# Optimization experiments

Measured on AMD Instinct MI355X. Metric: run time of the kernel, lower is better.

The kernel has to match this reference:

```python
import jax, jax.numpy as jnp
import numpy as np
from jax.scipy.linalg import solve_triangular

LS = 0.5414            # frozen GP length scale (_gp_scale.data = 0.5414)
L2 = LS * LS
D = 2
K_OPS = D + 2          # operators: identity, d/dx_i (i=1..d), laplacian
JITTER_KXX = 1e-5
JITTER_AKA = 1e-4
JITTER_YY = 1e-5


def _opiK(xout, xin, l2, d):
    # op_i applied to first arg of RBF kernel -> (bs, k, m, n)
    r = xout[:, :, None, :] - xin[:, None, :, :]            # (bs,m,n,d)
    u = jnp.sum(r * r, axis=-1) / l2                        # (bs,m,n)
    K = jnp.exp(-0.5 * u)
    ri = jnp.moveaxis(r, -1, 1)                             # (bs,d,m,n)
    grad = -(ri / l2) * K[:, None]                          # d/dx_i K
    lap = ((u - d) / l2) * K                                # Lap_x K
    return jnp.concatenate([K[:, None], grad, lap[:, None]], axis=1)


def _opiKopjfull(x, l2, d):
    # op_i on first arg, op_j on second arg -> (bs, k, k, m, m)
    r = x[:, :, None, :] - x[:, None, :, :]
    u = jnp.sum(r * r, axis=-1) / l2
    K = jnp.exp(-0.5 * u)
    ri = jnp.moveaxis(r, -1, 1)                             # (bs,d,m,m)
    gK = (ri / l2) * K[:, None]                             # d/dy_j K
    lapK = ((u - d) / l2) * K                               # Lap K (either arg)
    eye = jnp.eye(d, dtype=x.dtype)[None, :, :, None, None]
    gg = (eye / l2 - ri[:, :, None] * ri[:, None] / (l2 * l2)) * K[:, None, None]  # d/dx_i d/dy_j K
    glap = (ri / (l2 * l2)) * (((2.0 + d - u) * K)[:, None])  # d/dx_i Lap_y K
    laplap = (((u - d) ** 2 - 4.0 * u + 2.0 * d) / (l2 * l2)) * K  # Lap_x Lap_y K
    row0 = jnp.concatenate([K[:, None, None], gK[:, None], lapK[:, None, None]], axis=2)
    rowg = jnp.concatenate([(-gK)[:, :, None], gg, glap[:, :, None]], axis=2)
    rowl = jnp.concatenate([lapK[:, None, None], (-glap)[:, None], laplap[:, None, None]], axis=2)
    return jnp.concatenate([row0, rowg, rowl], axis=1)


def _psd_solve(L, B):
    # (Kxx + jitter I)^{-1} B via Cholesky (stands in for gpytorch inv_matmul/CG)
    y = solve_triangular(L, B, lower=True)
    return solve_triangular(L, y, lower=True, trans=1)


def _forward(xin, meanin, Kin, weight, bias):
    bs, n, c = meanin.shape
    d, k, l2 = D, K_OPS, L2
    xout, m = xin, n
    r = xin[:, :, None, :] - xin[:, None, :, :]
    Kxx = jnp.exp(-0.5 * jnp.sum(r * r, axis=-1) / l2)      # (bs,n,n)
    In = jnp.eye(n, dtype=xin.dtype)
    Lc = jnp.linalg.cholesky(Kxx + JITTER_KXX * In)
    opiKmn = _opiK(xout, xin, l2, d)                        # (bs,k,m,n)
    # posterior mean of op_i applied to the GP
    opimean = (opiKmn.reshape(bs, k * m, n) @ _psd_solve(Lc, meanin)).reshape(bs, k, m, c)
    Amean = jnp.transpose(opimean, (0, 2, 3, 1)).reshape(bs, m, c * k) @ weight.T + bias
    W = weight.reshape(-1, c, k)                            # (cout,c,k)
    W2 = jnp.einsum('oci,ocj->ij', W, W) / W.shape[0]       # (k,k)
    Kxxinvopi = jnp.swapaxes(
        _psd_solve(Lc, jnp.swapaxes(opiKmn.reshape(bs, k * m, n), 1, 2)), 1, 2)  # (bs,km,n)
    interp_weights = jnp.swapaxes(_psd_solve(Lc, Kin), 1, 2)                      # (bs,n,n)
    opi_interp = jnp.transpose((Kxxinvopi @ interp_weights).reshape(bs, k, m, n), (0, 2, 3, 1))  # (bs,m,n,k)
    Ak_interp = (opi_interp @ W2).reshape(bs, m, n * k)
    Im = jnp.eye(m, dtype=xin.dtype)
    AkinA = Ak_interp @ jnp.transpose(opiKmn, (0, 3, 1, 2)).reshape(bs, n * k, m) + JITTER_AKA * Im
    opiKxxxopj = jnp.transpose(
        (Kxxinvopi @ jnp.swapaxes(opiKmn.reshape(bs, k * m, n), 1, 2)).reshape(bs, k, m, k, m),
        (0, 1, 3, 2, 4))                                    # (bs,k,k,m,m)
    ijkyy = _opiKopjfull(xout, l2, d) - opiKxxxopj          # posterior cov of op_i f, op_j f
    AkAyy = jnp.einsum('bijmp,ij->bmp', ijkyy, W2) + JITTER_YY * Im
    full_AKA = AkinA + AkAyy
    return (xout, Amean, full_AKA)


def setup_inputs() -> dict:
    bs, n, cin, cout = 4, 576, 32, 64
    key = jax.random.key(0)
    k1, k2, k3, k4, k5 = jax.random.split(key, 5)
    xin = jax.random.uniform(k1, (bs, n, D), dtype=jnp.float32) * 6.0
    meanin = jax.random.normal(k2, (bs, n, cin), dtype=jnp.float32)
    A = jax.random.normal(k3, (bs, n, n), dtype=jnp.float32) / np.float32(np.sqrt(n))
    Kin = A @ jnp.swapaxes(A, 1, 2) + 0.1 * jnp.eye(n, dtype=jnp.float32)  # PSD covariance
    fan_in = cin * K_OPS
    weight = jax.random.normal(k4, (cout, fan_in), dtype=jnp.float32) / np.float32(np.sqrt(fan_in))
    bias = jax.random.normal(k5, (cout,), dtype=jnp.float32) * 0.01
    return {"xin": xin, "meanin": meanin, "Kin": Kin, "weight": weight, "bias": bias}


def reference(xin, meanin, Kin, weight, bias):
    return _forward(xin, meanin, Kin, weight, bias)
```

## Files before the change

kernel.cpp:

```cpp
#include <hip/hip_runtime.h>
#include <math.h>

#define NPTS 576
#define N2 331776
#define BSZ 4
#define NB 64
#define NT 9

#define INVL2 (1.0f/0.29311396f)

typedef __attribute__((ext_vector_type(8))) short short8v;
typedef __attribute__((ext_vector_type(16))) float f32x16;

__global__ void build_k(const float* __restrict__ xin,
                        float* __restrict__ Kxx, float* __restrict__ opiK,
                        float* __restrict__ out,
                        const float* __restrict__ w, float* __restrict__ W2) {
    int idx = blockIdx.x * 256 + threadIdx.x;
    if (idx < 4608) out[idx] = xin[idx];
    int b = idx / N2;
    int rem = idx - b * N2;
    int m = rem / NPTS;
    int nn = rem - m * NPTS;
    const float* xb = xin + (size_t)b * NPTS * 2;
// ... 87 lines not shown
                }
            }
            float tii = __shfl(tcol[i], base + i);
            v[i] = s / tii;
        }
        #pragma unroll
        for (int i = 0; i < 16; ++i) V[base + i][base + c] = v[i];
    }
    __syncthreads();
    const int PI[6] = {1,2,3,2,3,3};
    const int PJ[6] = {0,1,2,0,1,0};
    int rr16 = tid >> 4, cc16 = tid & 15;
    for (int p = 0; p < 6; ++p) {
        int I = PI[p], J = PJ[p];
        float s = 0.0f;
        for (int K = J; K < I; ++K)
            #pragma unroll
            for (int t = 0; t < 16; ++t)
                s += T[I*16+rr16][K*16+t] * V[K*16+t][J*16+cc16];
        tmp[rr16][cc16] = s;
        __syncthreads();
        float s2 = 0.0f;
        for (int t = 0; t <= rr16; ++t) s2 += V[I*16+rr16][I*16+t] * tmp[t][cc16];
        __syncthreads();
        V[I*16+rr16][J*16+cc16] = -s2;
        __syncthreads();
    }
}

__global__ void chol_diag0(const float* __restrict__ A, float* __restrict__ LinvKK) {
    int b = blockIdx.x;
    const float* Ab = A + (size_t)b * N2;
    __shared__ float T[NB][NB+1];
    __shared__ float V[NB][NB+1];
    __shared__ float tmp[16][17];
    int tid = threadIdx.x;
    for (int idx = tid; idx < NB*NB; idx += 256) {
        int r = idx >> 6, c = idx & 63;
        T[r][c] = Ab[(size_t)r * NPTS + c];
        V[r][c] = 0.0f;
    }
    __syncthreads();
    factor_invert_64(T, V, tmp, tid);
    float* Vg = LinvKK + (size_t)b * NT * NB * NB;
    for (int idx = tid; idx < NB*NB; idx += 256) Vg[idx] = V[idx >> 6][idx & 63];
}

__global__ __launch_bounds__(256)
void chol_step(float* __restrict__ A, float* __restrict__ LL,
               float* __restrict__ LinvKK, int kb) {
    int b = blockIdx.y;
    int p = blockIdx.x;
    int ir = 0;
    while (p >= ir + 1) { p -= ir + 1; ir++; }
    int ib = kb + 1 + ir, jb = kb + 1 + p;
    float* Ab = A + (size_t)b * N2;
    float* LLb = LL + (size_t)b * N2;
    __shared__ float Ai[NB][NB+1];
    __shared__ float Aj[NB][NB+1];
    __shared__ float Vs[NB][NB+1];
    __shared__ float tmp[16][17];
    int tid = threadIdx.x;
    int tx = tid & 15, ty = tid >> 4;
    const float* Vg = LinvKK + ((size_t)b * NT + kb) * NB * NB;
    bool diag = (ib == jb);
    for (int idx = tid; idx < NB*NB; idx += 256) {
        int r = idx >> 6, c = idx & 63;
        Ai[r][c] = Ab[(size_t)(ib*NB + r) * NPTS + kb*NB + c];
        Aj[r][c] = diag ? 0.0f : Ab[(size_t)(jb*NB + r) * NPTS + kb*NB + c];
        Vs[r][c] = Vg[idx];
    }
    float U[4][4];
    #pragma unroll
    for (int i = 0; i < 4; ++i)
        #pragma unroll
        for (int j = 0; j < 4; ++j)
            U[i][j] = Ab[(size_t)(ib*NB + ty*4+i) * NPTS + jb*NB + tx*4+j];
    __syncthreads();
    float Li[4][4] = {}, Lj[4][4] = {};
    for (int k = 0; k < NB; ++k) {
        float a[4], v[4];
        #pragma unroll
        for (int i = 0; i < 4; ++i) a[i] = Ai[ty*4+i][k];
        #pragma unroll
        for (int j = 0; j < 4; ++j) v[j] = Vs[tx*4+j][k];
        #pragma unroll
        for (int i = 0; i < 4; ++i)
            #pragma unroll
            for (int j = 0; j < 4; ++j) Li[i][j] += a[i] * v[j];
        if (!diag) {
            float aj[4];
            #pragma unroll
            for (int i = 0; i < 4; ++i) aj[i] = Aj[ty*4+i][k];
            #pragma unroll
            for (int i = 0; i < 4; ++i)
                #pragma unroll
                for (int j = 0; j < 4; ++j) Lj[i][j] += aj[i] * v[j];
        }
    }
    __syncthreads();
    #pragma unroll
    for (int i = 0; i < 4; ++i)
        #pragma unroll
        for (int j = 0; j < 4; ++j) {
            Ai[ty*4+i][tx*4+j] = Li[i][j];
            Aj[ty*4+i][tx*4+j] = diag ? Li[i][j] : Lj[i][j];
        }
    if (diag) {
        #pragma unroll
        for (int i = 0; i < 4; ++i)
            #pragma unroll
            for (int j = 0; j < 4; ++j)
                LLb[(size_t)(ib*NB + ty*4+i) * NPTS + kb*NB + tx*4+j] = Li[i][j];
    }
    __syncthreads();
    float s[4][4] = {};
    for (int k = 0; k < NB; ++k) {
        float a[4], v[4];
        #pragma unroll
        for (int i = 0; i < 4; ++i) a[i] = Ai[ty*4+i][k];
        #pragma unroll
        for (int j = 0; j < 4; ++j) v[j] = Aj[tx*4+j][k];
        #pragma unroll
        for (int i = 0; i < 4; ++i)
            #pragma unroll
            for (int j = 0; j < 4; ++j) s[i][j] += a[i] * v[j];
    }
    #pragma unroll
    for (int i = 0; i < 4; ++i)
        #pragma unroll
        for (int j = 0; j < 4; ++j) U[i][j] -= s[i][j];
    if (blockIdx.x != 0) {
        #pragma unroll
        for (int i = 0; i < 4; ++i)
            #pragma unroll
            for (int j = 0; j < 4; ++j)
                Ab[(size_t)(ib*NB + ty*4+i) * NPTS + jb*NB + tx*4+j] = U[i][j];
        return;
    }
    __syncthreads();
    #pragma unroll
    for (int i = 0; i < 4; ++i)
        #pragma unroll
        for (int j = 0; j < 4; ++j) Ai[ty*4+i][tx*4+j] = U[i][j];
    for (int idx = tid; idx < NB*NB; idx += 256) Aj[idx >> 6][idx & 63] = 0.0f;
    __syncthreads();
    factor_invert_64(Ai, Aj, tmp, tid);
    float* Vo = LinvKK + ((size_t)b * NT + (kb + 1)) * NB * NB;
    for (int idx = tid; idx < NB*NB; idx += 256) Vo[idx] = Aj[idx >> 6][idx & 63];
}

__global__ __launch_bounds__(256)
void trinv_blk(const float* __restrict__ L, const float* __restrict__ LinvKK,
               float* __restrict__ Linv) {
    int sp = blockIdx.x, jb = blockIdx.y, b = blockIdx.z;
    const float* Lb = L + (size_t)b * N2;
    float* Xg = Linv + (size_t)b * N2;
    const float* Vg = LinvKK + (size_t)b * NT * NB * NB;
    int c0 = jb * NB + sp * 16;

    __shared__ float LsT[64][72];
    __shared__ float Xc[576][20];
    __shared__ float Ss[64][20];
    __shared__ float Red[4][64][20];

    int tid = threadIdx.x;
    int kq = tid >> 6;
    int rg = (tid >> 2) & 15;
    int cg = tid & 3;
    int sr = tid >> 2, st0 = (tid & 3) * 16;

    float4 pf0, pf1, pf2, pf3;

#define TRINV_ISSUE_L(ibv, kbv)                                               \
    { const float* src_ = Lb + (size_t)((ibv) * NB + sr) * NPTS + (kbv) * NB + st0; \
      pf0 = *(const float4*)(src_ + 0);  pf1 = *(const float4*)(src_ + 4);    \
      pf2 = *(const float4*)(src_ + 8);  pf3 = *(const float4*)(src_ + 12); }

#define TRINV_ISSUE_V(ibv)                                                    \
    { const float* src_ = Vg + (size_t)(ibv) * NB * NB + sr * NB + st0;       \
      pf0 = *(const float4*)(src_ + 0);  pf1 = *(const float4*)(src_ + 4);    \
      pf2 = *(const float4*)(src_ + 8);  pf3 = *(const float4*)(src_ + 12); }

#define TRINV_COMMIT()                                                        \
    { LsT[st0 + 0][sr]  = pf0.x; LsT[st0 + 1][sr]  = pf0.y;                   \
      LsT[st0 + 2][sr]  = pf0.z; LsT[st0 + 3][sr]  = pf0.w;                   \
      LsT[st0 + 4][sr]  = pf1.x; LsT[st0 + 5][sr]  = pf1.y;                   \
      LsT[st0 + 6][sr]  = pf1.z; LsT[st0 + 7][sr]  = pf1.w;                   \
      LsT[st0 + 8][sr]  = pf2.x; LsT[st0 + 9][sr]  = pf2.y;                   \
      LsT[st0 + 10][sr] = pf2.z; LsT[st0 + 11][sr] = pf2.w;                   \
      LsT[st0 + 12][sr] = pf3.x; LsT[st0 + 13][sr] = pf3.y;                   \
      LsT[st0 + 14][sr] = pf3.z; LsT[st0 + 15][sr] = pf3.w; }

    {
        const float* Vjj = Vg + (size_t)jb * NB * NB;
        int r = tid >> 2, c4 = (tid & 3) * 4;
        float4 v = *(const float4*)(Vjj + r * NB + sp * 16 + c4);
        *(float4*)&Xc[r][c4] = v;
        *(float4*)(Xg + (size_t)(jb * NB + r) * NPTS + c0 + c4) = v;
    }
    if (jb + 1 < NT) TRINV_ISSUE_L(jb + 1, jb);
    __syncthreads();

    for (int ib = jb + 1; ib < NT; ++ib) {
        float acc[4][4] = {};
        for (int kb = jb; kb < ib; ++kb) {
            TRINV_COMMIT();
            __syncthreads();
            if (kb + 1 < ib) { TRINV_ISSUE_L(ib, kb + 1); }
            else             { TRINV_ISSUE_V(ib); }
            int xbase = (kb - jb) * 64;
            #pragma unroll
            for (int t = 0; t < 16; ++t) {
                int k = kq * 16 + t;
                float a4[4]; *(float4*)a4 = *(const float4*)&LsT[k][rg * 4];
                float x4[4]; *(float4*)x4 = *(const float4*)&Xc[xbase + k][cg * 4];
                #pragma unroll
                for (int i = 0; i < 4; ++i)
                    #pragma unroll
                    for (int j = 0; j < 4; ++j)
                        acc[i][j] += a4[i] * x4[j];
            }
            __syncthreads();
        }
        TRINV_COMMIT();
        #pragma unroll
        for (int i = 0; i < 4; ++i)
            *(float4*)&Red[kq][rg * 4 + i][cg * 4] = *(float4*)&acc[i][0];
        __syncthreads();
        {
            int r = tid >> 2, c4 = (tid & 3) * 4;
            float4 s0 = *(float4*)&Red[0][r][c4];
            float4 s1 = *(float4*)&Red[1][r][c4];
            float4 s2 = *(float4*)&Red[2][r][c4];
            float4 s3 = *(float4*)&Red[3][r][c4];
            float4 s; s.x = s0.x + s1.x + s2.x + s3.x;
            s.y = s0.y + s1.y + s2.y + s3.y;
            s.z = s0.z + s1.z + s2.z + s3.z;
            s.w = s0.w + s1.w + s2.w + s3.w;
            *(float4*)&Ss[r][c4] = s;
        }
        __syncthreads();
        if (ib + 1 < NT) TRINV_ISSUE_L(ib + 1, jb);
        float acc2[4][4] = {};
        #pragma unroll
        for (int t = 0; t < 16; ++t) {
            int k = kq * 16 + t;
            float a4[4]; *(float4*)a4 = *(const float4*)&LsT[k][rg * 4];
            float s4[4]; *(float4*)s4 = *(const float4*)&Ss[k][cg * 4];
            #pragma unroll
            for (int i = 0; i < 4; ++i)
                #pragma unroll
                for (int j = 0; j < 4; ++j)
                    acc2[i][j] += a4[i] * s4[j];
        }
        __syncthreads();
        #pragma unroll
        for (int i = 0; i < 4; ++i)
            *(float4*)&Red[kq][rg * 4 + i][cg * 4] = *(float4*)&acc2[i][0];
        __syncthreads();
        int obase = (ib - jb) * 64;
        {
            int r = tid >> 2, c4 = (tid & 3) * 4;
            float4 s0 = *(float4*)&Red[0][r][c4];
            float4 s1 = *(float4*)&Red[1][r][c4];
            float4 s2 = *(float4*)&Red[2][r][c4];
            float4 s3 = *(float4*)&Red[3][r][c4];
            float4 s; s.x = -(s0.x + s1.x + s2.x + s3.x);
            s.y = -(s0.y + s1.y + s2.y + s3.y);
            s.z = -(s0.z + s1.z + s2.z + s3.z);
            s.w = -(s0.w + s1.w + s2.w + s3.w);
            *(float4*)&Xc[obase + r][c4] = s;
            *(float4*)(Xg + (size_t)(ib * NB + r) * NPTS + c0 + c4) = s;
        }
        __syncthreads();
    }
#undef TRINV_ISSUE_L
#undef TRINV_ISSUE_V
#undef TRINV_COMMIT
}

__device__ inline void split3(float v, unsigned short& h0, unsigned short& h1,
                              unsigned short& h2) {
    unsigned u0 = __float_as_uint(v) & 0xffff0000u;
    float f0 = __uint_as_float(u0);
    float r1 = v - f0;
    unsigned u1 = __float_as_uint(r1) & 0xffff0000u;
    float f1 = __uint_as_float(u1);
    float r2 = r1 - f1;
    h0 = (unsigned short)(u0 >> 16);
    h1 = (unsigned short)(u1 >> 16);
    h2 = (unsigned short)((__float_as_uint(r2) + 0x8000u) >> 16);
}

__device__ inline void pack_store(unsigned short* dst, const unsigned short* v) {
    uint4 w;
    w.x = (unsigned)v[0] | ((unsigned)v[1] << 16);
    w.y = (unsigned)v[2] | ((unsigned)v[3] << 16);
    w.z = (unsigned)v[4] | ((unsigned)v[5] << 16);
    w.w = (unsigned)v[6] | ((unsigned)v[7] << 16);
    *(uint4*)dst = w;
}

template<int EPIB>
__global__ __launch_bounds__(256, 2)
void mm_p2_mfma(const float* __restrict__ Aall, const float* __restrict__ Ball,
                float* __restrict__ Call, long sA, long sB, long sC)
{
    int id = blockIdx.x;
    int x8 = id & 7, qq = id >> 3;
    int nx = qq % 9;
    int band = x8 + 8 * (qq / 9);
    if (band >= 18 * BSZ) return;
    int t  = band % 18;
    int b  = band / 18;
    int pp = t / 9, my = t % 9;
    const float* A0 = Aall + (size_t)b * sA + (size_t)(pp * 2) * N2;
    const float* A1 = A0 + N2;
    const float* B  = Ball + (size_t)b * sB;
    float* C0 = Call + (size_t)b * sC + (size_t)(pp * 2) * N2;
    float* C1 = C0 + N2;
    int n0 = nx * 64, m0 = my * 64;

    __shared__ __align__(16) unsigned short As[12][2][64][8];
    __shared__ __align__(16) unsigned short Bs[6][2][64][8];

    int tid  = threadIdx.x;
    int lane = tid & 63;
    int wid  = tid >> 6;
    int wr = wid >> 1, wc = wid & 1;

    f32x16 acc0, acc1;
    #pragma unroll
    for (int i = 0; i < 16; ++i) { acc0[i] = 0.0f; acc1[i] = 0.0f; }

    int ap   = tid >> 7;
    int aq   = tid & 127;
    int ar   = aq >> 1;
    int asub = aq & 1;
    const float* Apl = ap ? A1 : A0;
    int areg = ar >> 5;
    int aln  = ar & 31;

    int bc   = tid & 63;
    int bkg  = tid >> 6;
    int bsub = bkg >> 1;
    int bln  = (bc & 31) + 32 * (bkg & 1);
    int bwc  = bc >> 5;

    float av[16];
    float bv[8];

    auto loadA = [&](int k0) {
        const float* p = Apl + (size_t)(m0 + ar) * 576 + k0 + asub * 16;
        float4 t0 = *(const float4*)(p);
        float4 t1 = *(const float4*)(p + 4);
        float4 t2 = *(const float4*)(p + 8);
        float4 t3 = *(const float4*)(p + 12);
        av[0]=t0.x;  av[1]=t0.y;  av[2]=t0.z;  av[3]=t0.w;
        av[4]=t1.x;  av[5]=t1.y;  av[6]=t1.z;  av[7]=t1.w;
        av[8]=t2.x;  av[9]=t2.y;  av[10]=t2.z; av[11]=t2.w;
        av[12]=t3.x; av[13]=t3.y; av[14]=t3.z; av[15]=t3.w;
    };
    auto loadB = [&](int k0) {
        const float* p = B + (size_t)(k0 + bkg * 8) * 576 + n0 + bc;
        #pragma unroll
        for (int j = 0; j < 8; ++j) {
            float v = p[(size_t)j * 576];
            if (EPIB) { if (k0 + bkg * 8 + j == n0 + bc) v -= 1.0f; }
            bv[j] = v;
        }
    };
    auto storeA = [&]() {
        unsigned short s0[16], s1[16], s2[16];
        #pragma unroll
        for (int j = 0; j < 16; ++j) split3(av[j], s0[j], s1[j], s2[j]);
        #pragma unroll
        for (int h = 0; h < 2; ++h) {
            int ln = aln + 32 * h;
            pack_store(&As[(ap*3 + 0)*2 + areg][asub][ln][0], &s0[8*h]);
            pack_store(&As[(ap*3 + 1)*2 + areg][asub][ln][0], &s1[8*h]);
            pack_store(&As[(ap*3 + 2)*2 + areg][asub][ln][0], &s2[8*h]);
        }
    };
    auto storeB = [&]() {
        unsigned short s0[8], s1[8], s2[8];
        #pragma unroll
        for (int j = 0; j < 8; ++j) split3(bv[j], s0[j], s1[j], s2[j]);
        pack_store(&Bs[0*2 + bwc][bsub][bln][0], s0);
        pack_store(&Bs[1*2 + bwc][bsub][bln][0], s1);
        pack_store(&Bs[2*2 + bwc][bsub][bln][0], s2);
    };

    const short8v* Af = (const short8v*)As;
    const short8v* Bf = (const short8v*)Bs;

    loadA(0); loadB(0);
    for (int k0 = 0; k0 < 576; k0 += 32) {
        storeA(); storeB();
        __syncthreads();
        if (k0 + 32 < 576) { loadA(k0 + 32); loadB(k0 + 32); }
        #pragma unroll
        for (int sub = 0; sub < 2; ++sub) {
            short8v b0 = Bf[((0*2 + wc)*2 + sub)*64 + lane];
            short8v b1 = Bf[((1*2 + wc)*2 + sub)*64 + lane];
            short8v b2 = Bf[((2*2 + wc)*2 + sub)*64 + lane];
            short8v a0 = Af[((0*3 + 0)*2 + wr)*128 + sub*64 + lane];
            short8v a1 = Af[((0*3 + 1)*2 + wr)*128 + sub*64 + lane];
            short8v a2 = Af[((0*3 + 2)*2 + wr)*128 + sub*64 + lane];
            acc0 = __builtin_amdgcn_mfma_f32_32x32x16_bf16(a0, b0, acc0, 0, 0, 0);
            acc0 = __builtin_amdgcn_mfma_f32_32x32x16_bf16(a0, b1, acc0, 0, 0, 0);
            acc0 = __builtin_amdgcn_mfma_f32_32x32x16_bf16(a1, b0, acc0, 0, 0, 0);
            acc0 = __builtin_amdgcn_mfma_f32_32x32x16_bf16(a1, b1, acc0, 0, 0, 0);
            acc0 = __builtin_amdgcn_mfma_f32_32x32x16_bf16(a0, b2, acc0, 0, 0, 0);
            acc0 = __builtin_amdgcn_mfma_f32_32x32x16_bf16(a2, b0, acc0, 0, 0, 0);
            a0 = Af[((1*3 + 0)*2 + wr)*128 + sub*64 + lane];
            a1 = Af[((1*3 + 1)*2 + wr)*128 + sub*64 + lane];
            a2 = Af[((1*3 + 2)*2 + wr)*128 + sub*64 + lane];
            acc1 = __builtin_amdgcn_mfma_f32_32x32x16_bf16(a0, b0, acc1, 0, 0, 0);
            acc1 = __builtin_amdgcn_mfma_f32_32x32x16_bf16(a0, b1, acc1, 0, 0, 0);
            acc1 = __builtin_amdgcn_mfma_f32_32x32x16_bf16(a1, b0, acc1, 0, 0, 0);
            acc1 = __builtin_amdgcn_mfma_f32_32x32x16_bf16(a1, b1, acc1, 0, 0, 0);
            acc1 = __builtin_amdgcn_mfma_f32_32x32x16_bf16(a0, b2, acc1, 0, 0, 0);
            acc1 = __builtin_amdgcn_mfma_f32_32x32x16_bf16(a2, b0, acc1, 0, 0, 0);
        }
        __syncthreads();
    }

    int colg = n0 + 32*wc + (lane & 31);
    int rowb = m0 + 32*wr + 4*(lane >> 5);
    #pragma unroll
    for (int reg = 0; reg < 16; ++reg) {
        int row = rowb + (reg & 3) + 8*(reg >> 2);
        C0[(size_t)row * 576 + colg] = acc0[reg];
        C1[(size_t)row * 576 + colg] = acc1[reg];
    }
}

__global__ __launch_bounds__(256, 2)
void mm_abt_mfma(const float* __restrict__ Aall, const float* __restrict__ Ball,
                 float* __restrict__ Call, long sA, long sB, long sC, long sSplit)
{
    int p = blockIdx.x;
    int ir = 0;
    while (p >= ir + 1) { p -= ir + 1; ir++; }
    int my = ir, nx = p;
    int zz = blockIdx.z;
    int sp = zz & 3, b = zz >> 2;
    const float* A = Aall + (size_t)b * sA + (size_t)sp * N2;
    const float* B = Ball + (size_t)b * sB + (size_t)sp * N2;
    float* Cp = Call + (size_t)b * sC + (size_t)sp * sSplit;
    int m0 = my * 64, n0 = nx * 64;

    __shared__ __align__(16) unsigned short Fr[12][2][64][8];

    int tid  = threadIdx.x;
    int lane = tid & 63;
    int wid  = tid >> 6;
    int wr = wid >> 1, wc = wid & 1;

    f32x16 acc;
    #pragma unroll
    for (int i = 0; i < 16; ++i) acc[i] = 0.0f;

    int sel  = tid >> 7;
    int q2   = tid & 127;
    int r    = q2 >> 1;
    int ssub = q2 & 1;
    const float* Src = sel ? B : A;
    int base0 = sel ? n0 : m0;
    int rreg = r >> 5;
    int rln  = r & 31;

    float av[16];

    auto loadF = [&](int k0) {
        const float* pp = Src + (size_t)(base0 + r) * 576 + k0 + ssub * 16;
        float4 t0 = *(const float4*)(pp);
        float4 t1 = *(const float4*)(pp + 4);
        float4 t2 = *(const float4*)(pp + 8);
        float4 t3 = *(const float4*)(pp + 12);
        av[0]=t0.x;  av[1]=t0.y;  av[2]=t0.z;  av[3]=t0.w;
        av[4]=t1.x;  av[5]=t1.y;  av[6]=t1.z;  av[7]=t1.w;
        av[8]=t2.x;  av[9]=t2.y;  av[10]=t2.z; av[11]=t2.w;
        av[12]=t3.x; av[13]=t3.y; av[14]=t3.z; av[15]=t3.w;
    };
    auto storeF = [&]() {
        unsigned short s0[16], s1[16], s2[16];
        #pragma unroll
        for (int j = 0; j < 16; ++j) split3(av[j], s0[j], s1[j], s2[j]);
        #pragma unroll
        for (int h = 0; h < 2; ++h) {
            int ln = rln + 32 * h;
            pack_store(&Fr[sel*6 + 0*2 + rreg][ssub][ln][0], &s0[8*h]);
            pack_store(&Fr[sel*6 + 1*2 + rreg][ssub][ln][0], &s1[8*h]);
            pack_store(&Fr[sel*6 + 2*2 + rreg][ssub][ln][0], &s2[8*h]);
        }
    };

    const short8v* Ff = (const short8v*)Fr;

    loadF(0);
    for (int k0 = 0; k0 < 576; k0 += 32) {
        storeF();
        __syncthreads();
        if (k0 + 32 < 576) loadF(k0 + 32);
        #pragma unroll
        for (int sub = 0; sub < 2; ++sub) {
            short8v a0 = Ff[((0*2 + wr)*2 + sub)*64 + lane];
            short8v a1 = Ff[((1*2 + wr)*2 + sub)*64 + lane];
            short8v a2 = Ff[((2*2 + wr)*2 + sub)*64 + lane];
            short8v b0 = Ff[((6 + 0*2 + wc)*2 + sub)*64 + lane];
            short8v b1 = Ff[((6 + 1*2 + wc)*2 + sub)*64 + lane];
            short8v b2 = Ff[((6 + 2*2 + wc)*2 + sub)*64 + lane];
            acc = __builtin_amdgcn_mfma_f32_32x32x16_bf16(a0, b0, acc, 0, 0, 0);
            acc = __builtin_amdgcn_mfma_f32_32x32x16_bf16(a0, b1, acc, 0, 0, 0);
            acc = __builtin_amdgcn_mfma_f32_32x32x16_bf16(a1, b0, acc, 0, 0, 0);
            acc = __builtin_amdgcn_mfma_f32_32x32x16_bf16(a1, b1, acc, 0, 0, 0);
            acc = __builtin_amdgcn_mfma_f32_32x32x16_bf16(a0, b2, acc, 0, 0, 0);
            acc = __builtin_amdgcn_mfma_f32_32x32x16_bf16(a2, b0, acc, 0, 0, 0);
        }
        __syncthreads();
    }

    int colg = n0 + 32*wc + (lane & 31);
    int rowb = m0 + 32*wr + 4*(lane >> 5);
    #pragma unroll
    for (int reg = 0; reg < 16; ++reg) {
        int row = rowb + (reg & 3) + 8*(reg >> 2);
        Cp[(size_t)row * 576 + colg] = acc[reg];
    }
}

__global__ __launch_bounds__(256, 2)
void mm_ata_mfma(const float* __restrict__ Lg, float* __restrict__ C,
                 long sA, long sC)
{
    int p = blockIdx.x;
    int ir = 0;
    while (p >= ir + 1) { p -= ir + 1; ir++; }
    int my = ir, nx = p;
    int b = blockIdx.z;
    const float* A = Lg + (size_t)b * sA;
    float* Cb = C + (size_t)b * sC;
    int m0 = my * 64, n0 = nx * 64;
    int kBeg = m0;

    __shared__ __align__(16) unsigned short Fr[12][2][64][8];

    int tid  = threadIdx.x;
    int lane = tid & 63;
    int wid  = tid >> 6;
    int wr = wid >> 1, wc = wid & 1;

    f32x16 acc;
    #pragma unroll
    for (int i = 0; i < 16; ++i) acc[i] = 0.0f;

    int sel  = tid >> 7;
    int q2   = tid & 127;
    int col  = q2 & 63;
    int ssub = q2 >> 6;
    int c0base = sel ? n0 : m0;
    int rreg = col >> 5;
    int rln  = col & 31;

    float av[16];

    auto loadF = [&](int k0) {
        const float* pp = A + (size_t)(k0 + ssub * 16) * 576 + c0base + col;
        #pragma unroll
        for (int j = 0; j < 16; ++j) av[j] = pp[(size_t)j * 576];
    };
    auto storeF = [&]() {
        unsigned short s0[16], s1[16], s2[16];
        #pragma unroll
        for (int j = 0; j < 16; ++j) split3(av[j], s0[j], s1[j], s2[j]);
        #pragma unroll
        for (int h = 0; h < 2; ++h) {
            int ln = rln + 32 * h;
            pack_store(&Fr[sel*6 + 0*2 + rreg][ssub][ln][0], &s0[8*h]);
            pack_store(&Fr[sel*6 + 1*2 + rreg][ssub][ln][0], &s1[8*h]);
            pack_store(&Fr[sel*6 + 2*2 + rreg][ssub][ln][0], &s2[8*h]);
        }
    };

    const short8v* Ff = (const short8v*)Fr;

    loadF(kBeg);
    for (int k0 = kBeg; k0 < 576; k0 += 32) {
        storeF();
        __syncthreads();
        if (k0 + 32 < 576) loadF(k0 + 32);
        #pragma unroll
        for (int sub = 0; sub < 2; ++sub) {
            short8v a0 = Ff[((0*2 + wr)*2 + sub)*64 + lane];
            short8v a1 = Ff[((1*2 + wr)*2 + sub)*64 + lane];
            short8v a2 = Ff[((2*2 + wr)*2 + sub)*64 + lane];
            short8v b0 = Ff[((6 + 0*2 + wc)*2 + sub)*64 + lane];
            short8v b1 = Ff[((6 + 1*2 + wc)*2 + sub)*64 + lane];
            short8v b2 = Ff[((6 + 2*2 + wc)*2 + sub)*64 + lane];
            acc = __builtin_amdgcn_mfma_f32_32x32x16_bf16(a0, b0, acc, 0, 0, 0);
            acc = __builtin_amdgcn_mfma_f32_32x32x16_bf16(a0, b1, acc, 0, 0, 0);
            acc = __builtin_amdgcn_mfma_f32_32x32x16_bf16(a1, b0, acc, 0, 0, 0);
            acc = __builtin_amdgcn_mfma_f32_32x32x16_bf16(a1, b1, acc, 0, 0, 0);
            acc = __builtin_amdgcn_mfma_f32_32x32x16_bf16(a0, b2, acc, 0, 0, 0);
            acc = __builtin_amdgcn_mfma_f32_32x32x16_bf16(a2, b0, acc, 0, 0, 0);
        }
        __syncthreads();
    }

    int colg = n0 + 32*wc + (lane & 31);
    int rowb = m0 + 32*wr + 4*(lane >> 5);
    #pragma unroll
    for (int reg = 0; reg < 16; ++reg) {
        int row = rowb + (reg & 3) + 8*(reg >> 2);
        float v = acc[reg];
        Cb[(size_t)row * 576 + colg] = v;
        Cb[(size_t)colg * 576 + row] = v;
    }
}

__global__ __launch_bounds__(256, 2)
void mm_ab_mfma(const float* __restrict__ Aall, const float* __restrict__ Ball,
                float* __restrict__ Call, long sA, long sB, long sC)
{
    int nx = blockIdx.x % 9, my = blockIdx.x / 9;
    int b = blockIdx.z;
    const float* A = Aall + (size_t)b * sA;
    const float* B = Ball + (size_t)b * sB;
    float* Cb = Call + (size_t)b * sC;
    int m0 = my * 64, n0 = nx * 64;

    __shared__ __align__(16) unsigned short Fr[12][2][64][8];

    int tid  = threadIdx.x;
    int lane = tid & 63;
    int wid  = tid >> 6;
    int wr = wid >> 1, wc = wid & 1;

    f32x16 acc;
    #pragma unroll
    for (int i = 0; i < 16; ++i) acc[i] = 0.0f;

    int sel  = tid >> 7;
    int q2   = tid & 127;
    int ar   = q2 >> 1;
    int asub = q2 & 1;
    int areg = ar >> 5, aln = ar & 31;
    int bcol = q2 & 63;
    int bssub = q2 >> 6;
    int breg = bcol >> 5, brln = bcol & 31;

    float av[16];

    auto loadF = [&](int k0) {
        if (sel == 0) {
            const float* pp = A + (size_t)(m0 + ar) * 576 + k0 + asub * 16;
            float4 t0 = *(const float4*)(pp);
            float4 t1 = *(const float4*)(pp + 4);
            float4 t2 = *(const float4*)(pp + 8);
            float4 t3 = *(const float4*)(pp + 12);
            av[0]=t0.x;  av[1]=t0.y;  av[2]=t0.z;  av[3]=t0.w;
            av[4]=t1.x;  av[5]=t1.y;  av[6]=t1.z;  av[7]=t1.w;
            av[8]=t2.x;  av[9]=t2.y;  av[10]=t2.z; av[11]=t2.w;
            av[12]=t3.x; av[13]=t3.y; av[14]=t3.z; av[15]=t3.w;
        } else {
            const float* pp = B + (size_t)(k0 + bssub * 16) * 576 + n0 + bcol;
            #pragma unroll
            for (int j = 0; j < 16; ++j) av[j] = pp[(size_t)j * 576];
        }
    };
    auto storeF = [&]() {
        unsigned short s0[16], s1[16], s2[16];
        #pragma unroll
        for (int j = 0; j < 16; ++j) split3(av[j], s0[j], s1[j], s2[j]);
        int reg0 = sel ? (6 + 0*2 + breg) : (0*2 + areg);
        int reg1 = sel ? (6 + 1*2 + breg) : (1*2 + areg);
        int reg2 = sel ? (6 + 2*2 + breg) : (2*2 + areg);
        int sb   = sel ? bssub : asub;
        int ln0  = sel ? brln : aln;
        #pragma unroll
        for (int h = 0; h < 2; ++h) {
            int ln = ln0 + 32 * h;
            pack_store(&Fr[reg0][sb][ln][0], &s0[8*h]);
            pack_store(&Fr[reg1][sb][ln][0], &s1[8*h]);
            pack_store(&Fr[reg2][sb][ln][0], &s2[8*h]);
        }
    };

    const short8v* Ff = (const short8v*)Fr;

    loadF(0);
    for (int k0 = 0; k0 < 576; k0 += 32) {
        storeF();
        __syncthreads();
        if (k0 + 32 < 576) loadF(k0 + 32);
        #pragma unroll
        for (int sub = 0; sub < 2; ++sub) {
            short8v a0 = Ff[((0*2 + wr)*2 + sub)*64 + lane];
            short8v a1 = Ff[((1*2 + wr)*2 + sub)*64 + lane];
            short8v a2 = Ff[((2*2 + wr)*2 + sub)*64 + lane];
            short8v b0 = Ff[((6 + 0*2 + wc)*2 + sub)*64 + lane];
            short8v b1 = Ff[((6 + 1*2 + wc)*2 + sub)*64 + lane];
            short8v b2 = Ff[((6 + 2*2 + wc)*2 + sub)*64 + lane];
            acc = __builtin_amdgcn_mfma_f32_32x32x16_bf16(a0, b0, acc, 0, 0, 0);
            acc = __builtin_amdgcn_mfma_f32_32x32x16_bf16(a0, b1, acc, 0, 0, 0);
            acc = __builtin_amdgcn_mfma_f32_32x32x16_bf16(a1, b0, acc, 0, 0, 0);
            acc = __builtin_amdgcn_mfma_f32_32x32x16_bf16(a1, b1, acc, 0, 0, 0);
            acc = __builtin_amdgcn_mfma_f32_32x32x16_bf16(a0, b2, acc, 0, 0, 0);
            acc = __builtin_amdgcn_mfma_f32_32x32x16_bf16(a2, b0, acc, 0, 0, 0);
        }
        __syncthreads();
    }

    int colg = n0 + 32*wc + (lane & 31);
    int rowb = m0 + 32*wr + 4*(lane >> 5);
    #pragma unroll
    for (int reg = 0; reg < 16; ++reg) {
        int row = rowb + (reg & 3) + 8*(reg >> 2);
        Cb[(size_t)row * 576 + colg] = acc[reg];
    }
}

template<int TA, int TB, int SK, int TRI, int SWZ, int EPIB, int TRIC>
__global__ __launch_bounds__(256)
void mm_kernel(const float* __restrict__ Aall, const float* __restrict__ Ball,
               float* __restrict__ Call,
               int M, int N, int K, int planeK,
               int lda, int ldb, int ldc,
               long sA, long sB, long sC, long pA, long pB, long sSplit, int MT)
{
    int nx, my, zz;
    if (TRIC) {
        int p = blockIdx.x;
        int ir = 0;
        while (p >= ir + 1) { p -= ir + 1; ir++; }
        my = ir; nx = p; zz = blockIdx.z;
    } else if (SWZ) {
        int id = blockIdx.x;
        int x8 = id & 7;
        int q  = id >> 3;
        nx = q % 9;
        int band = x8 + 8 * (q / 9);
        if (band >= MT * 4 * SK) return;
        my = band % MT;
        zz = band / MT;
    } else { nx = blockIdx.x; my = blockIdx.y; zz = blockIdx.z; }
    int sp = (SK > 1) ? (zz % SK) : 0;
    int b  = (SK > 1) ? (zz / SK) : zz;
    const float* A = Aall + (size_t)b * sA;
    const float* B = Ball + (size_t)b * sB;
    float* C = Call + (size_t)b * sC + (size_t)sp * sSplit;
    int n0 = nx * 64;
    int m0 = my * 64;

    __shared__ float As[16][68];
    __shared__ float Bs[16][68];

    int tid = threadIdx.x;
    int tx = tid & 15, ty = tid >> 4;

    float acc[4][4] = {};
    bool mFull = (m0 + 64 <= M);
    bool nFull = (n0 + 64 <= N);

    int triBeg = 0;
    if (TRI) { int mx = (m0 > n0 ? m0 : n0); triBeg = mx & ~15; }
    int kBeg = triBeg, kEnd = K;
    if (SK > 1) {
        int len = K - triBeg;
        int chunk = ((len / SK) + 15) & ~15;
        kBeg = triBeg + sp * chunk;
        if (kBeg > K) kBeg = K;
        kEnd = (sp == SK - 1) ? K : (kBeg + chunk < K ? kBeg + chunk : K);
    }

    float avr[4];
    float bvr[4];

    auto loadA = [&](int k0) {
        int plane = k0 / planeK;
        int koff  = k0 - plane * planeK;
        if (TA == 0) {
            const float* Ab = A + (size_t)pA * plane;
            int r = tid >> 2, c4 = (tid & 3) * 4;
            int gm = m0 + r;
            if (mFull || gm < M) {
                float4 t = *(const float4*)(Ab + (size_t)gm * lda + koff + c4);
                avr[0]=t.x; avr[1]=t.y; avr[2]=t.z; avr[3]=t.w;
            } else { avr[0]=avr[1]=avr[2]=avr[3]=0.0f; }
        } else {
            int r = tid >> 4, c4 = (tid & 15) * 4;
            const float* p = A + (size_t)(koff + r) * lda + m0 + c4;
            if (mFull) {
                float4 t = *(const float4*)p;
                avr[0]=t.x; avr[1]=t.y; avr[2]=t.z; avr[3]=t.w;
            } else {
                #pragma unroll
                for (int jj = 0; jj < 4; ++jj)
                    avr[jj] = (m0 + c4 + jj < M) ? p[jj] : 0.0f;
            }
        }
    };
    auto storeA = [&]() {
        if (TA == 0) {
            int r = tid >> 2, c4 = (tid & 3) * 4;
            #pragma unroll
            for (int q = 0; q < 4; ++q) As[c4+q][r] = avr[q];
        } else {
            int r = tid >> 4, c4 = (tid & 15) * 4;
            #pragma unroll
            for (int q = 0; q < 4; ++q) As[r][c4+q] = avr[q];
        }
    };
    auto loadB = [&](int k0) {
        int plane = k0 / planeK;
        int koff  = k0 - plane * planeK;
        if (TB == 0) {
            int r = tid >> 4, c4 = (tid & 15) * 4;
            const float* p = B + (size_t)(koff + r) * ldb + n0 + c4;
            if (nFull) {
                float4 t = *(const float4*)p;
                bvr[0]=t.x; bvr[1]=t.y; bvr[2]=t.z; bvr[3]=t.w;
            } else {
                #pragma unroll
                for (int jj = 0; jj < 4; ++jj)
                    bvr[jj] = (n0 + c4 + jj < N) ? p[jj] : 0.0f;
            }
            if (EPIB) {
                int gk = koff + r;
                #pragma unroll
                for (int jj = 0; jj < 4; ++jj)
                    if (gk == n0 + c4 + jj) bvr[jj] -= 1.0f;
            }
        } else {
            const float* Bb = B + (size_t)pB * plane;
            int r = tid >> 2, c4 = (tid & 3) * 4;
            int gp = n0 + r;
            if (nFull || gp < N) {
                float4 t = *(const float4*)(Bb + (size_t)gp * ldb + koff + c4);
                bvr[0]=t.x; bvr[1]=t.y; bvr[2]=t.z; bvr[3]=t.w;
            } else { bvr[0]=bvr[1]=bvr[2]=bvr[3]=0.0f; }
        }
    };
    auto storeB = [&]() {
        if (TB == 0) {
            int r = tid >> 4, c4 = (tid & 15) * 4;
            #pragma unroll
            for (int q = 0; q < 4; ++q) Bs[r][c4+q] = bvr[q];
        } else {
            int r = tid >> 2, c4 = (tid & 3) * 4;
            #pragma unroll
            for (int q = 0; q < 4; ++q) Bs[c4+q][r] = bvr[q];
        }
    };

    if (kBeg < kEnd) {
        loadA(kBeg); loadB(kBeg);
        for (int k0 = kBeg; k0 < kEnd; k0 += 16) {
            storeA(); storeB();
            __syncthreads();
            if (k0 + 16 < kEnd) { loadA(k0 + 16); loadB(k0 + 16); }
            #pragma unroll
            for (int kk = 0; kk < 16; ++kk) {
                float a[4], bb[4];
                *(float4*)a  = *(const float4*)&As[kk][ty*4];
                *(float4*)bb = *(const float4*)&Bs[kk][tx*4];
                #pragma unroll
                for (int i = 0; i < 4; ++i)
                    #pragma unroll
                    for (int j = 0; j < 4; ++j)
                        acc[i][j] += a[i] * bb[j];
            }
            __syncthreads();
        }
    }

    #pragma unroll
    for (int i = 0; i < 4; ++i) {
        int gm = m0 + ty*4 + i;
        if (gm >= M) continue;
        #pragma unroll
        for (int j = 0; j < 4; ++j) {
            int gn = n0 + tx*4 + j;
            if (gn >= N) continue;
            C[(size_t)gm * ldc + gn] = acc[i][j];
        }
    }
}

__global__ void combine_solm4(const float* __restrict__ p, float* __restrict__ o) {
    int i = blockIdx.x * 256 + threadIdx.x;
    o[i] = p[i] + p[i + 73728] + p[i + 2*73728] + p[i + 3*73728];
}

__global__ void combine_prior4_sym(const float* __restrict__ p0,
                                   const float* __restrict__ xin,
                                   const float* __restrict__ W2g,
                                   float* __restrict__ o, long stride) {
    __shared__ float w[16];
    int tid = threadIdx.x;
    if (tid < 16) w[tid] = W2g[tid];
    __syncthreads();
    int idx = blockIdx.x * 256 + tid;
    int b = idx / N2;
    int rem = idx - b * N2;
    int m = rem / NPTS, n = rem - m * NPTS;
    if (m < n) return;
    const float* xb = xin + (size_t)b * NPTS * 2;
    float r0 = xb[m*2+0] - xb[n*2+0];
    float r1 = xb[m*2+1] - xb[n*2+1];
    float u = (r0*r0 + r1*r1) * INVL2;
    float Kv = expf(-0.5f * u);
    float i2 = INVL2 * INVL2;
    float gK0 = r0 * INVL2 * Kv;
    float gK1 = r1 * INVL2 * Kv;
    float lapK = (u - 2.0f) * INVL2 * Kv;
    float gg00 = (INVL2 - r0*r0*i2) * Kv;
    float gg01 = (-r0*r1*i2) * Kv;
    float gg11 = (INVL2 - r1*r1*i2) * Kv;
    float gl0 = r0 * i2 * (4.0f - u) * Kv;
    float gl1 = r1 * i2 * (4.0f - u) * Kv;
    float ll = ((u-2.0f)*(u-2.0f) - 4.0f*u + 4.0f) * i2 * Kv;
    float prior =
          w[0]*Kv + w[1]*gK0 + w[2]*gK1 + w[3]*lapK
        + w[4]*(-gK0) + w[5]*gg00 + w[6]*gg01 + w[7]*gl0
        + w[8]*(-gK1) + w[9]*gg01 + w[10]*gg11 + w[11]*gl1
        + w[12]*lapK + w[13]*(-gl0) + w[14]*(-gl1) + w[15]*ll;
    float v = p0[idx] + p0[idx + stride] + p0[idx + 2*stride] + p0[idx + 3*stride]
            + prior;
    if (m == n) v += 1.1e-4f;
    o[(size_t)b * N2 + (size_t)m * NPTS + n] = v;
    if (m != n)
        o[(size_t)b * N2 + (size_t)n * NPTS + m] = v;
}

__global__ void opiw2_k(const float* __restrict__ opiK, const float* __restrict__ W2,
                        float* __restrict__ outB) {
    int idx = blockIdx.x * 256 + threadIdx.x;
    int b = idx / N2;
    int rem = idx - b * N2;
    size_t base = (size_t)b * 4 * N2 + rem;
    float k0 = opiK[base], k1 = opiK[base + N2], k2 = opiK[base + 2*N2], k3 = opiK[base + 3*N2];
    #pragma unroll
    for (int i = 0; i < 4; ++i)
        outB[base + (size_t)i * N2] = W2[i*4+0]*k0 + W2[i*4+1]*k1 + W2[i*4+2]*k2 + W2[i*4+3]*k3;
}

__global__ __launch_bounds__(256)
void amean_k(const float* __restrict__ opimean, const float* __restrict__ weight,
             const float* __restrict__ bias, float* __restrict__ out) {
    int b = blockIdx.y;
    int m0 = blockIdx.x * 32;
    __shared__ float Wl[64][128];
    __shared__ float om[32][128];
    int tid = threadIdx.x;
    for (int idx = tid; idx < 64*128; idx += 256) Wl[idx / 128][idx & 127] = weight[idx];
    for (int idx = tid; idx < 32*128; idx += 256) {
        int m = idx >> 7, ck = idx & 127, c = ck >> 2, kop = ck & 3;
        om[m][ck] = opimean[((size_t)b * 4 + kop) * NPTS * 32 + (size_t)(m0 + m) * 32 + c];
    }
    __syncthreads();
    int ml = tid >> 3, o0 = (tid & 7) * 8;
    float acc[8] = {};
    for (int ck = 0; ck < 128; ++ck) {
        float v = om[ml][ck];
        #pragma unroll
        for (int q = 0; q < 8; ++q) acc[q] += v * Wl[o0+q][ck];
    }
    #pragma unroll
    for (int q = 0; q < 8; ++q)
        out[4608 + ((size_t)b * NPTS + m0 + ml) * 64 + o0 + q] = acc[q] + bias[o0+q];
}

static inline int gridSwz(int MT, int Z) { return 8 * 9 * ((MT * Z + 7) / 8); }

extern "C" void kernel_launch(void* const* d_in, const int* in_sizes, int n_in,
                              void* d_out, int out_size, void* d_ws, size_t ws_size,
                              hipStream_t stream) {
    const float* xin    = (const float*)d_in[0];
    const float* meanin = (const float*)d_in[1];
    const float* Kin    = (const float*)d_in[2];
    const float* weight = (const float*)d_in[3];
    const float* bias   = (const float*)d_in[4];
    float* out = (float*)d_out;
    float* ws  = (float*)d_ws;

    const long N2L = N2;
    float* W2      = ws;
    float* LinvKK  = ws + 64;
    float* R1 = LinvKK + 147456;
    float* R2 = R1 + 4*N2L;
    float* R3 = R2 + 4*N2L;
    float* R4 = R3 + 4*N2L;
    float* R5 = R4 + 16*N2L;
    float* R6 = R5 + 16*N2L;

    hipMemsetAsync(R2, 0, (size_t)4 * N2 * sizeof(float), stream);
    build_k<<<dim3((BSZ*N2)/256), dim3(256), 0, stream>>>(
        xin, R1, R4, out, weight, W2);
    chol_diag0<<<dim3(BSZ), dim3(256), 0, stream>>>(R1, LinvKK);
    for (int kb = 0; kb < NT - 1; ++kb) {
        int t = NT - 1 - kb;
        chol_step<<<dim3(t*(t+1)/2, BSZ), dim3(256), 0, stream>>>(R1, R3, LinvKK, kb);
    }
    trinv_blk<<<dim3(4, NT, BSZ), dim3(256), 0, stream>>>(R3, LinvKK, R2);
    mm_ata_mfma<<<dim3(45, 1, BSZ), dim3(256), 0, stream>>>(R2, R3, N2L, N2L);
    mm_kernel<0,0,4,0,0,0,0><<<dim3(1,9,16), dim3(256), 0, stream>>>(
        R3, meanin, R6, 576,32,576,576, 576,32,32,
        N2L,18432,18432, 0,0, 73728, 9);
    combine_solm4<<<dim3(288), dim3(256), 0, stream>>>(R6, R2);
    mm_kernel<0,0,1,0,0,0,0><<<dim3(1,36,BSZ), dim3(256), 0, stream>>>(
        R4, R2, R2 + 73728, 2304,32,576,576, 576,32,32,
        4*N2L,18432,73728, 0,0, 0, 9);
    amean_k<<<dim3(18,BSZ), dim3(256), 0, stream>>>(R2 + 73728, weight, bias, out);
    mm_ab_mfma<<<dim3(81, 1, BSZ), dim3(256), 0, stream>>>(
        Kin, R3, R1, N2L, N2L, N2L);
    mm_p2_mfma<0><<<dim3(gridSwz(18,4)), dim3(256), 0, stream>>>(
        R4, R3, R5, 4*N2L, N2L, 4*N2L);
    opiw2_k<<<dim3((BSZ*N2)/256), dim3(256), 0, stream>>>(R4, W2, R4);
    mm_p2_mfma<1><<<dim3(gridSwz(18,4)), dim3(256), 0, stream>>>(
        R5, R1, R6, 4*N2L, N2L, 4*N2L);
    mm_abt_mfma<<<dim3(45,1,BSZ*4), dim3(256), 0, stream>>>(
        R6, R4, R5, 4*N2L, 4*N2L, N2L, 4*N2L);
    combine_prior4_sym<<<dim3(5184), dim3(256), 0, stream>>>(
        R5, xin, W2, out + 152064, 4*N2L);
}
```

Baseline: 857.9 us.

## Process four operator planes per block and pre-split B into bf16 triples

```diff
diff --git a/kernel.cpp b/kernel.cpp
--- a/kernel.cpp
+++ b/kernel.cpp
@@ -413,27 +413,40 @@
     *(uint4*)dst = w;
 }
 
-template<int EPIB>
+__global__ void presplit_b(const float* __restrict__ In,
+                           unsigned short* __restrict__ Sp) {
+    int idx = blockIdx.x * 256 + threadIdx.x;
+    int b = idx / N2;
+    int rem = idx - b * N2;
+    float v = In[(size_t)b * N2 + rem];
+    unsigned short h0, h1, h2;
+    split3(v, h0, h1, h2);
+    size_t base = (size_t)b * 3 * N2 + rem;
+    Sp[base]          = h0;
+    Sp[base + N2]     = h1;
+    Sp[base + 2*N2]   = h2;
+}
+
+template<int EPIB, int PSB>
 __global__ __launch_bounds__(256, 2)
-void mm_p2_mfma(const float* __restrict__ Aall, const float* __restrict__ Ball,
+void mm_p4_mfma(const float* __restrict__ Aall, const float* __restrict__ Ball,
+                const unsigned short* __restrict__ Bspall,
                 float* __restrict__ Call, long sA, long sB, long sC)
 {
     int id = blockIdx.x;
     int x8 = id & 7, qq = id >> 3;
     int nx = qq % 9;
     int band = x8 + 8 * (qq / 9);
-    if (band >= 18 * BSZ) return;
-    int t  = band % 18;
-    int b  = band / 18;
-    int pp = t / 9, my = t % 9;
-    const float* A0 = Aall + (size_t)b * sA + (size_t)(pp * 2) * N2;
-    const float* A1 = A0 + N2;
-    const float* B  = Ball + (size_t)b * sB;
-    float* C0 = Call + (size_t)b * sC + (size_t)(pp * 2) * N2;
-    float* C1 = C0 + N2;
+    if (band >= 9 * BSZ) return;
+    int my = band % 9;
+    int b  = band / 9;
+    const float* Ab = Aall + (size_t)b * sA;
+    const float* B  = PSB ? nullptr : (Ball + (size_t)b * sB);
+    const unsigned short* Bsp = PSB ? (Bspall + (size_t)b * 3 * N2) : nullptr;
+    float* Cb = Call + (size_t)b * sC;
     int n0 = nx * 64, m0 = my * 64;
 
-    __shared__ __align__(16) unsigned short As[12][2][64][8];
+    __shared__ __align__(16) unsigned short As[24][2][64][8];
     __shared__ __align__(16) unsigned short Bs[6][2][64][8];
 
     int tid  = threadIdx.x;
@@ -441,66 +454,74 @@
     int wid  = tid >> 6;
     int wr = wid >> 1, wc = wid & 1;
 
-    f32x16 acc0, acc1;
-    #pragma unroll
-    for (int i = 0; i < 16; ++i) { acc0[i] = 0.0f; acc1[i] = 0.0f; }
-
-    int ap   = tid >> 7;
-    int aq   = tid & 127;
-    int ar   = aq >> 1;
-    int asub = aq & 1;
-    const float* Apl = ap ? A1 : A0;
-    int areg = ar >> 5;
-    int aln  = ar & 31;
-
-    int bc   = tid & 63;
-    int bkg  = tid >> 6;
-    int bsub = bkg >> 1;
-    int bln  = (bc & 31) + 32 * (bkg & 1);
-    int bwc  = bc >> 5;
-
-    float av[16];
+    f32x16 acc[4];
+    #pragma unroll
+    for (int p = 0; p < 4; ++p)
+        #pragma unroll
+        for (int i = 0; i < 16; ++i) acc[p][i] = 0.0f;
+
+    int apl = tid >> 6;
+    int ar  = tid & 63;
+    int areg = ar >> 5, aln = ar & 31;
+    int bc = tid & 63, bkg = tid >> 6;
+    int bsub = bkg >> 1, bln = (bc & 31) + 32 * (bkg & 1), bwc = bc >> 5;
+
+    float av[32];
     float bv[8];
+    short8v bsp0, bsp1, bsp2;
 
     auto loadA = [&](int k0) {
-        const float* p = Apl + (size_t)(m0 + ar) * 576 + k0 + asub * 16;
-        float4 t0 = *(const float4*)(p);
-        float4 t1 = *(const float4*)(p + 4);
-        float4 t2 = *(const float4*)(p + 8);
-        float4 t3 = *(const float4*)(p + 12);
-        av[0]=t0.x;  av[1]=t0.y;  av[2]=t0.z;  av[3]=t0.w;
-        av[4]=t1.x;  av[5]=t1.y;  av[6]=t1.z;  av[7]=t1.w;
-        av[8]=t2.x;  av[9]=t2.y;  av[10]=t2.z; av[11]=t2.w;
-        av[12]=t3.x; av[13]=t3.y; av[14]=t3.z; av[15]=t3.w;
+        const float* p = Ab + (size_t)apl * N2 + (size_t)(m0 + ar) * 576 + k0;
+        #pragma unroll
+        for (int q = 0; q < 8; ++q) {
+            float4 t = *(const float4*)(p + q * 4);
+            av[q*4+0]=t.x; av[q*4+1]=t.y; av[q*4+2]=t.z; av[q*4+3]=t.w;
+        }
+    };
+    auto storeA = [&]() {
+        unsigned short s0[32], s1[32], s2[32];
+        #pragma unroll
+        for (int j = 0; j < 32; ++j) split3(av[j], s0[j], s1[j], s2[j]);
+        #pragma unroll
+        for (int sub = 0; sub < 2; ++sub)
+            #pragma unroll
+            for (int h = 0; h < 2; ++h) {
+                int ln = aln + 32 * h;
+                int o = sub * 16 + 8 * h;
+                pack_store(&As[(apl*3 + 0)*2 + areg][sub][ln][0], &s0[o]);
+                pack_store(&As[(apl*3 + 1)*2 + areg][sub][ln][0], &s1[o]);
+                pack_store(&As[(apl*3 + 2)*2 + areg][sub][ln][0], &s2[o]);
+            }
     };
     auto loadB = [&](int k0) {
-        const float* p = B + (size_t)(k0 + bkg * 8) * 576 + n0 + bc;
-        #pragma unroll
-        for (int j = 0; j < 8; ++j) {
-            float v = p[(size_t)j * 576];
-            if (EPIB) { if (k0 + bkg * 8 + j == n0 + bc) v -= 1.0f; }
-            bv[j] = v;
-        }
-    };
-    auto storeA = [&]() {
-        unsigned short s0[16], s1[16], s2[16];
-        #pragma unroll
-        for (int j = 0; j < 16; ++j) split3(av[j], s0[j], s1[j], s2[j]);
-        #pragma unroll
-        for (int h = 0; h < 2; ++h) {
-            int ln = aln + 32 * h;
-            pack_store(&As[(ap*3 + 0)*2 + areg][asub][ln][0], &s0[8*h]);
-            pack_store(&As[(ap*3 + 1)*2 + areg][asub][ln][0], &s1[8*h]);
-            pack_store(&As[(ap*3 + 2)*2 + areg][asub][ln][0], &s2[8*h]);
+        if (PSB) {
+            const unsigned short* p = Bsp + (size_t)(n0 + bc) * 576 + k0 + bkg * 8;
+            bsp0 = *(const short8v*)(p);
+            bsp1 = *(const short8v*)(p + N2);
+            bsp2 = *(const short8v*)(p + 2*N2);
+        } else {
+            const float* p = B + (size_t)(k0 + bkg * 8) * 576 + n0 + bc;
+            #pragma unroll
+            for (int j = 0; j < 8; ++j) {
+                float v = p[(size_t)j * 576];
+                if (EPIB) { if (k0 + bkg * 8 + j == n0 + bc) v -= 1.0f; }
+                bv[j] = v;
+            }
         }
     };
     auto storeB = [&]() {
-        unsigned short s0[8], s1[8], s2[8];
-        #pragma unroll
-        for (int j = 0; j < 8; ++j) split3(bv[j], s0[j], s1[j], s2[j]);
-        pack_store(&Bs[0*2 + bwc][bsub][bln][0], s0);
-        pack_store(&Bs[1*2 + bwc][bsub][bln][0], s1);
-        pack_store(&Bs[2*2 + bwc][bsub][bln][0], s2);
+        if (PSB) {
+            *(short8v*)&Bs[0*2 + bwc][bsub][bln][0] = bsp0;
+            *(short8v*)&Bs[1*2 + bwc][bsub][bln][0] = bsp1;
+            *(short8v*)&Bs[2*2 + bwc][bsub][bln][0] = bsp2;
+        } else {
+            unsigned short s0[8], s1[8], s2[8];
+            #pragma unroll
+            for (int j = 0; j < 8; ++j) split3(bv[j], s0[j], s1[j], s2[j]);
+            pack_store(&Bs[0*2 + bwc][bsub][bln][0], s0);
+            pack_store(&Bs[1*2 + bwc][bsub][bln][0], s1);
+            pack_store(&Bs[2*2 + bwc][bsub][bln][0], s2);
+        }
     };
 
     const short8v* Af = (const short8v*)As;
@@ -516,24 +537,18 @@
             short8v b0 = Bf[((0*2 + wc)*2 + sub)*64 + lane];
             short8v b1 = Bf[((1*2 + wc)*2 + sub)*64 + lane];
             short8v b2 = Bf[((2*2 + wc)*2 + sub)*64 + lane];
-            short8v a0 = Af[((0*3 + 0)*2 + wr)*128 + sub*64 + lane];
-            short8v a1 = Af[((0*3 + 1)*2 + wr)*128 + sub*64 + lane];
-            short8v a2 = Af[((0*3 + 2)*2 + wr)*128 + sub*64 + lane];
-            acc0 = __builtin_amdgcn_mfma_f32_32x32x16_bf16(a0, b0, acc0, 0, 0, 0);
-            acc0 = __builtin_amdgcn_mfma_f32_32x32x16_bf16(a0, b1, acc0, 0, 0, 0);
-            acc0 = __builtin_amdgcn_mfma_f32_32x32x16_bf16(a1, b0, acc0, 0, 0, 0);
-            acc0 = __builtin_amdgcn_mfma_f32_32x32x16_bf16(a1, b1, acc0, 0, 0, 0);
-            acc0 = __builtin_amdgcn_mfma_f32_32x32x16_bf16(a0, b2, acc0, 0, 0, 0);
-            acc0 = __builtin_amdgcn_mfma_f32_32x32x16_bf16(a2, b0, acc0, 0, 0, 0);
-            a0 = Af[((1*3 + 0)*2 + wr)*128 + sub*64 + lane];
-            a1 = Af[((1*3 + 1)*2 + wr)*128 + sub*64 + lane];
-            a2 = Af[((1*3 + 2)*2 + wr)*128 + sub*64 + lane];
-            acc1 = __builtin_amdgcn_mfma_f32_32x32x16_bf16(a0, b0, acc1, 0, 0, 0);
-            acc1 = __builtin_amdgcn_mfma_f32_32x32x16_bf16(a0, b1, acc1, 0, 0, 0);
-            acc1 = __builtin_amdgcn_mfma_f32_32x32x16_bf16(a1, b0, acc1, 0, 0, 0);
-            acc1 = __builtin_amdgcn_mfma_f32_32x32x16_bf16(a1, b1, acc1, 0, 0, 0);
-            acc1 = __builtin_amdgcn_mfma_f32_32x32x16_bf16(a0, b2, acc1, 0, 0, 0);
-            acc1 = __builtin_amdgcn_mfma_f32_32x32x16_bf16(a2, b0, acc1, 0, 0, 0);
+            #pragma unroll
+            for (int pl = 0; pl < 4; ++pl) {
+                short8v a0 = Af[(((pl*3 + 0)*2 + wr)*2 + sub)*64 + lane];
+                short8v a1 = Af[(((pl*3 + 1)*2 + wr)*2 + sub)*64 + lane];
+                short8v a2 = Af[(((pl*3 + 2)*2 + wr)*2 + sub)*64 + lane];
+                acc[pl] = __builtin_amdgcn_mfma_f32_32x32x16_bf16(a0, b0, acc[pl], 0, 0, 0);
+                acc[pl] = __builtin_amdgcn_mfma_f32_32x32x16_bf16(a0, b1, acc[pl], 0, 0, 0);
+                acc[pl] = __builtin_amdgcn_mfma_f32_32x32x16_bf16(a1, b0, acc[pl], 0, 0, 0);
+                acc[pl] = __builtin_amdgcn_mfma_f32_32x32x16_bf16(a1, b1, acc[pl], 0, 0, 0);
+                acc[pl] = __builtin_amdgcn_mfma_f32_32x32x16_bf16(a0, b2, acc[pl], 0, 0, 0);
+                acc[pl] = __builtin_amdgcn_mfma_f32_32x32x16_bf16(a2, b0, acc[pl], 0, 0, 0);
+            }
         }
         __syncthreads();
     }
@@ -541,10 +556,13 @@
     int colg = n0 + 32*wc + (lane & 31);
     int rowb = m0 + 32*wr + 4*(lane >> 5);
     #pragma unroll
-    for (int reg = 0; reg < 16; ++reg) {
-        int row = rowb + (reg & 3) + 8*(reg >> 2);
-        C0[(size_t)row * 576 + colg] = acc0[reg];
-        C1[(size_t)row * 576 + colg] = acc1[reg];
+    for (int pl = 0; pl < 4; ++pl) {
+        float* Cp = Cb + (size_t)pl * N2;
+        #pragma unroll
+        for (int reg = 0; reg < 16; ++reg) {
+            int row = rowb + (reg & 3) + 8*(reg >> 2);
+            Cp[(size_t)row * 576 + colg] = acc[pl][reg];
+        }
     }
 }
 
@@ -1122,17 +1140,19 @@
         R3, meanin, R6, 576,32,576,576, 576,32,32,
         N2L,18432,18432, 0,0, 73728, 9);
     combine_solm4<<<dim3(288), dim3(256), 0, stream>>>(R6, R2);
+    presplit_b<<<dim3((BSZ*N2)/256), dim3(256), 0, stream>>>(
+        R3, (unsigned short*)R6);
     mm_kernel<0,0,1,0,0,0,0><<<dim3(1,36,BSZ), dim3(256), 0, stream>>>(
         R4, R2, R2 + 73728, 2304,32,576,576, 576,32,32,
         4*N2L,18432,73728, 0,0, 0, 9);
     amean_k<<<dim3(18,BSZ), dim3(256), 0, stream>>>(R2 + 73728, weight, bias, out);
     mm_ab_mfma<<<dim3(81, 1, BSZ), dim3(256), 0, stream>>>(
         Kin, R3, R1, N2L, N2L, N2L);
-    mm_p2_mfma<0><<<dim3(gridSwz(18,4)), dim3(256), 0, stream>>>(
-        R4, R3, R5, 4*N2L, N2L, 4*N2L);
+    mm_p4_mfma<0,1><<<dim3(gridSwz(9,4)), dim3(256), 0, stream>>>(
+        R4, nullptr, (const unsigned short*)R6, R5, 4*N2L, 0, 4*N2L);
     opiw2_k<<<dim3((BSZ*N2)/256), dim3(256), 0, stream>>>(R4, W2, R4);
-    mm_p2_mfma<1><<<dim3(gridSwz(18,4)), dim3(256), 0, stream>>>(
-        R5, R1, R6, 4*N2L, N2L, 4*N2L);
+    mm_p4_mfma<1,0><<<dim3(gridSwz(9,4)), dim3(256), 0, stream>>>(
+        R5, R1, nullptr, R6, 4*N2L, N2L, 4*N2L);
     mm_abt_mfma<<<dim3(45,1,BSZ*4), dim3(256), 0, stream>>>(
         R6, R4, R5, 4*N2L, 4*N2L, N2L, 4*N2L);
     combine_prior4_sym<<<dim3(5184), dim3(256), 0, stream>>>(
```

Measured after the change: 897.9 us. 1.05x slower.
